# Performance work log

Measured on AMD Instinct MI355X. Metric: run time of the kernel, lower is better.

Reference implementation:

```python
import jax, jax.numpy as jnp
import numpy as np

N, E = 50000, 800000
IN, HID, HEADS, OUT = 128, 32, 8, 40
D1 = HID * HEADS  # 256


def setup_inputs() -> dict:
    key = jax.random.key(0)
    ks = jax.random.split(key, 24)

    def w(k, fin, fout):
        return (jax.random.normal(k, (fin, fout), jnp.float32) / np.sqrt(fin)).astype(jnp.float32)

    def b(k, fout):
        return (jax.random.normal(k, (fout,), jnp.float32) * 0.02).astype(jnp.float32)

    inp = {
        "x": jax.random.normal(ks[0], (N, IN), jnp.float32),
        "edge_index": jax.random.randint(ks[1], (2, E), 0, N, dtype=jnp.int64),
        # layer 1: TransformerConv(IN -> HID, heads=HEADS, concat=True, beta=True)
        "q1w": w(ks[2], IN, D1), "q1b": b(ks[3], D1),
        "k1w": w(ks[4], IN, D1), "k1b": b(ks[5], D1),
        "v1w": w(ks[6], IN, D1), "v1b": b(ks[7], D1),
        "s1w": w(ks[8], IN, D1), "s1b": b(ks[9], D1),
        "b1w": w(ks[10], 3 * D1, 1),
        # layer 2: TransformerConv(D1 -> OUT, heads=1, concat=False, beta=True)
        "q2w": w(ks[11], D1, OUT), "q2b": b(ks[12], OUT),
        "k2w": w(ks[13], D1, OUT), "k2b": b(ks[14], OUT),
        "v2w": w(ks[15], D1, OUT), "v2b": b(ks[16], OUT),
        "s2w": w(ks[17], D1, OUT), "s2b": b(ks[18], OUT),
        "b2w": w(ks[19], 3 * OUT, 1),
    }
    return inp


def _tconv(x, src, dst, qw, qb, kw, kb, vw, vb, sw, sb, bw, heads, ch, concat):
    """PyG TransformerConv (no edge_attr, root_weight=True, beta=True), eval mode."""
    n = x.shape[0]
    q = (x @ qw + qb).reshape(n, heads, ch)
    k = (x @ kw + kb).reshape(n, heads, ch)
    v = (x @ vw + vb).reshape(n, heads, ch)
    # per-edge attention logits: message flows src(j) -> dst(i)
    alpha = jnp.einsum("ehc,ehc->eh", q[dst], k[src]) / np.sqrt(ch)  # [E,H]
    # segment softmax over incoming edges of each dst node
    amax = jax.ops.segment_max(alpha, dst, num_segments=n)  # [N,H]
    a = jnp.exp(alpha - amax[dst])
    asum = jax.ops.segment_sum(a, dst, num_segments=n)  # [N,H]
    attn = a / asum[dst]  # [E,H]
    # scatter-aggregate weighted values
    out = jax.ops.segment_sum(v[src] * attn[:, :, None], dst, num_segments=n)  # [N,H,C]
    out = out.reshape(n, heads * ch) if concat else out.mean(axis=1)
    skip = x @ sw + sb
    beta = jax.nn.sigmoid(jnp.concatenate([out, skip, out - skip], axis=-1) @ bw)  # [N,1]
    return beta * skip + (1.0 - beta) * out


def reference(x, edge_index, q1w, q1b, k1w, k1b, v1w, v1b, s1w, s1b, b1w,
              q2w, q2b, k2w, k2b, v2w, v2b, s2w, s2b, b2w):
    src, dst = edge_index[0], edge_index[1]
    h = jax.nn.elu(_tconv(x, src, dst, q1w, q1b, k1w, k1b, v1w, v1b, s1w, s1b, b1w, HEADS, HID, True))
    return _tconv(h, src, dst, q2w, q2b, k2w, k2b, v2w, v2b, s2w, s2b, b2w, 1, OUT, False)
```

## Files before the change

### kernel.cpp

```cpp
#include <hip/hip_runtime.h>
#include <cstdint>
#include <cstddef>

#define N_NODES 50000
#define N_EDGES 800000
#define IN_F    128
#define HID     32
#define HEADS   8
#define OUT_F   40
#define D1      256
#define W1COLS  1024
#define W2COLS  160
#define CAP     64

#define GFILL_B   3125
#define G1_BX     391
#define G1_BY     8
#define G1_GEMM_B (G1_BX * G1_BY)
#define G1_TOTAL  (GFILL_B + G1_GEMM_B)

typedef unsigned short ushortT;
typedef unsigned char  ucharT;
typedef unsigned short ushortx8 __attribute__((ext_vector_type(8)));
typedef __bf16 bf16x8 __attribute__((ext_vector_type(8)));
typedef float floatx4 __attribute__((ext_vector_type(4)));
typedef float floatx2 __attribute__((ext_vector_type(2)));

__device__ inline ushortT f2bf(float f) {
    union { float f; unsigned int u; } c; c.f = f;
    unsigned int r = c.u + 0x7FFFu + ((c.u >> 16) & 1u);
    return (ushortT)(r >> 16);
}
__device__ inline float bf2f(ushortT h) {
    union { unsigned int u; float f; } c; c.u = ((unsigned int)h) << 16; return c.f;
}

#define PREP_CONV_B  6250
#define PREP_W1_B    512
#define PREP_W2_B    160
#define PREP_TOTAL_B (PREP_CONV_B + PREP_W1_B + PREP_W2_B)

__global__ __launch_bounds__(256) void k_prep(
        const float* __restrict__ x, ushortT* __restrict__ xb,
        const float* __restrict__ q1w, const float* __restrict__ k1w,
        const float* __restrict__ v1w, const float* __restrict__ s1w,
        const float* __restrict__ q1b, const float* __restrict__ k1b,
        const float* __restrict__ v1b, const float* __restrict__ s1b,
        ushortT* __restrict__ W1T, float* __restrict__ b1c,
        const float* __restrict__ q2w, const float* __restrict__ k2w,
        const float* __restrict__ v2w, const float* __restrict__ s2w,
        const float* __restrict__ q2b, const float* __restrict__ k2b,
        const float* __restrict__ v2b, const float* __restrict__ s2b,
        ushortT* __restrict__ W2T, float* __restrict__ b2c) {
    int b = blockIdx.x;
    int tid = threadIdx.x;
    if (b < PREP_CONV_B) {
        int i = b * 256 + tid;
        float4 v = reinterpret_cast<const float4*>(x)[i];
        ushort4 o;
        o.x = f2bf(v.x); o.y = f2bf(v.y); o.z = f2bf(v.z); o.w = f2bf(v.w);
        reinterpret_cast<ushort4*>(xb)[i] = o;
    } else if (b < PREP_CONV_B + PREP_W1_B) {
        int t = (b - PREP_CONV_B) * 256 + tid;
        int c = t / IN_F, k = t % IN_F;
        int sel = c >> 8, cc = c & 255;
        const float* w = sel == 0 ? q1w : sel == 1 ? k1w : sel == 2 ? v1w : s1w;
        W1T[(size_t)c * IN_F + k] = f2bf(w[(size_t)k * D1 + cc]);
        if (k == 0) {
            const float* bb = sel == 0 ? q1b : sel == 1 ? k1b : sel == 2 ? v1b : s1b;
            b1c[c] = bb[cc];
        }
    } else {
        int t = (b - PREP_CONV_B - PREP_W1_B) * 256 + tid;
        int c = t / D1, k = t % D1;
        int sel = c / OUT_F, cc = c % OUT_F;
        const float* w = sel == 0 ? q2w : sel == 1 ? k2w : sel == 2 ? v2w : s2w;
        W2T[(size_t)c * D1 + k] = f2bf(w[(size_t)k * OUT_F + cc]);
        if (k == 0) {
            const float* bb = sel == 0 ? q2b : sel == 1 ? k2b : sel == 2 ? v2b : s2b;
            b2c[c] = bb[cc];
        }
    }
}

template<int MODE>
__global__ __launch_bounds__(256) void gemm_mfma_pack(
        const ushortT* __restrict__ A, const ushortT* __restrict__ BT,
        const float* __restrict__ bias, float* __restrict__ QSf,
        ushortT* __restrict__ QSh, ucharT* __restrict__ KV8,
        ushortT* __restrict__ K2V2,
        const int* __restrict__ ei, int* __restrict__ cursor, int* __restrict__ col,
        int M, int K, int Nn) {
    constexpr int TM = 128, TN = 128, TK = 64, LDP = 72;
    __shared__ ushortT As[TM * LDP];
    __shared__ ushortT Bs[TN * LDP];
    int bx2, by2;
    if (MODE == 1) {
        int t = blockIdx.x;
        int idx;
        bool isFill;
        if (t < 2 * GFILL_B) { isFill = !(t & 1); idx = t >> 1; }
        else                 { isFill = false;    idx = t - GFILL_B; }
        if (isFill) {
            int e = idx * 256 + threadIdx.x;
            if (e < N_EDGES) {
                int dd = ei[N_EDGES + e];
                int p = atomicAdd(&cursor[dd], 1);
                col[dd * CAP + p] = ei[e];
            }
            return;
        }
        bx2 = idx % G1_BX;
        by2 = idx / G1_BX;
    } else {
        bx2 = blockIdx.x;
        by2 = blockIdx.y;
    }
    int tid = threadIdx.x;
    int lane = tid & 63, wave = tid >> 6;
    int bm = bx2 * TM, bn = by2 * TN;
    int wm = (wave & 1) * 64, wn = (wave >> 1) * 64;
    int mrow = lane & 15, g = lane >> 4;
    floatx4 acc[4][4] = {};

    for (int k0 = 0; k0 < K; k0 += TK) {
#pragma unroll
        for (int it = 0; it < 4; ++it) {
            int idx = tid + it * 256;
            int r = idx >> 3, c = (idx & 7) * 8;
            int gm = bm + r;
            ushortx8 val;
            if (gm < M) val = *reinterpret_cast<const ushortx8*>(A + (size_t)gm * K + k0 + c);
            else        val = (ushortx8)0;
            *reinterpret_cast<ushortx8*>(As + r * LDP + c) = val;
        }
#pragma unroll
        for (int it = 0; it < 4; ++it) {
            int idx = tid + it * 256;
            int r = idx >> 3, c = (idx & 7) * 8;
            int gn = bn + r;
            ushortx8 val;
            if (gn < Nn) val = *reinterpret_cast<const ushortx8*>(BT + (size_t)gn * K + k0 + c);
            else         val = (ushortx8)0;
            *reinterpret_cast<ushortx8*>(Bs + r * LDP + c) = val;
        }
        __syncthreads();
#pragma unroll
        for (int kc = 0; kc < TK / 32; ++kc) {
            bf16x8 a[4], b[4];
#pragma unroll
            for (int i = 0; i < 4; ++i)
                a[i] = *reinterpret_cast<const bf16x8*>(As + (wm + i * 16 + mrow) * LDP + kc * 32 + g * 8);
#pragma unroll
            for (int j = 0; j < 4; ++j)
                b[j] = *reinterpret_cast<const bf16x8*>(Bs + (wn + j * 16 + mrow) * LDP + kc * 32 + g * 8);
#pragma unroll
            for (int i = 0; i < 4; ++i)
#pragma unroll
                for (int j = 0; j < 4; ++j)
                    acc[i][j] = __builtin_amdgcn_mfma_f32_16x16x32_bf16(a[i], b[j], acc[i][j], 0, 0, 0);
        }
        __syncthreads();
    }

    if (MODE == 1) {
        float* lds = reinterpret_cast<float*>(As) + wave * 1088;
        int sec = by2 >> 1;
        int ccbase = (by2 & 1) * 128 + wn;
        int cb4 = (lane & 15) * 4;
        int rlo = lane >> 4;
        float4 bv = *reinterpret_cast<const float4*>(bias + by2 * 128 + wn + cb4);
#pragma unroll
        for (int i = 0; i < 4; ++i) {
#pragma unroll
            for (int j = 0; j < 4; ++j)
#pragma unroll
                for (int r = 0; r < 4; ++r)
                    lds[(g * 4 + r) * 68 + j * 16 + mrow] = acc[i][j][r];
#pragma unroll
            for (int it = 0; it < 4; ++it) {
                int row = it * 4 + rlo;
                int gm = bm + wm + i * 16 + row;
                if (gm >= M) continue;
                float4 v = *reinterpret_cast<float4*>(lds + row * 68 + cb4);
                v.x += bv.x; v.y += bv.y; v.z += bv.z; v.w += bv.w;
                int cc = ccbase + cb4;
                if (sec == 0 || sec == 3) {
                    ushort4 h;
                    h.x = f2bf(v.x); h.y = f2bf(v.y); h.z = f2bf(v.z); h.w = f2bf(v.w);
                    ushortT* dst = QSh + (size_t)gm * 512 + (sec == 3 ? 256 : 0) + cc;
                    *reinterpret_cast<ushort4*>(dst) = h;
                } else {
                    unsigned int pk = 0;
                    pk = __builtin_amdgcn_cvt_pk_fp8_f32(v.x, v.y, pk, false);
                    pk = __builtin_amdgcn_cvt_pk_fp8_f32(v.z, v.w, pk, true);
                    ucharT* dst = KV8 + (size_t)gm * 512 + (sec == 2 ? 256 : 0) + cc;
                    *reinterpret_cast<unsigned int*>(dst) = pk;
                }
            }
        }
    } else {
#pragma unroll
        for (int i = 0; i < 4; ++i) {
#pragma unroll
            for (int j = 0; j < 4; ++j) {
                int gn = bn + wn + j * 16 + mrow;
                if (gn >= Nn) continue;
                float bvs = bias[gn];
#pragma unroll
                for (int r = 0; r < 4; ++r) {
                    int gm = bm + wm + i * 16 + g * 4 + r;
                    if (gm >= M) continue;
                    float val = acc[i][j][r] + bvs;
                    int sec = gn / OUT_F, cc = gn % OUT_F;
                    if (sec == 0)      QSf[(size_t)gm * 80 + cc] = val;
                    else if (sec == 1) K2V2[(size_t)gm * 80 + cc] = f2bf(val);
                    else if (sec == 2) K2V2[(size_t)gm * 80 + 40 + cc] = f2bf(val);
                    else               QSf[(size_t)gm * 80 + 40 + cc] = val;
                }
            }
        }
    }
}

__global__ __launch_bounds__(256) void k_edge1(
        const ushortT* __restrict__ QSh, const ucharT* __restrict__ KV8,
        const float* __restrict__ bw,
        const int* __restrict__ degc, const int* __restrict__ col,
        ushortT* __restrict__ H1b) {
    int gid  = blockIdx.x * blockDim.x + threadIdx.x;
    int node = gid >> 6;
    int lane = threadIdx.x & 63;
    if (node >= N_NODES) return;
    const float scale = 0.17677669529663687f;
    ushort4 qh = *reinterpret_cast<const ushort4*>(QSh + (size_t)node * 512 + lane * 4);
    float4 q;
    q.x = bf2f(qh.x) * scale; q.y = bf2f(qh.y) * scale;
    q.z = bf2f(qh.z) * scale; q.w = bf2f(qh.w) * scale;

    float l = 0.f;
    float4 acc = make_float4(0.f, 0.f, 0.f, 0.f);
    int start = node * CAP;
    int d = degc[node];
    int t = 0;
    for (; t + 2 <= d; t += 2) {
        int j0 = col[start + t];
        int j1 = col[start + t + 1];
        const ucharT* row0 = KV8 + (size_t)j0 * 512 + lane * 4;
        const ucharT* row1 = KV8 + (size_t)j1 * 512 + lane * 4;
        unsigned int ku0 = *reinterpret_cast<const unsigned int*>(row0);
        unsigned int vu0 = *reinterpret_cast<const unsigned int*>(row0 + 256);
        unsigned int ku1 = *reinterpret_cast<const unsigned int*>(row1);
        unsigned int vu1 = *reinterpret_cast<const unsigned int*>(row1 + 256);
        floatx2 k0a = __builtin_amdgcn_cvt_pk_f32_fp8(ku0, false);
        floatx2 k0b = __builtin_amdgcn_cvt_pk_f32_fp8(ku0, true);
        floatx2 k1a = __builtin_amdgcn_cvt_pk_f32_fp8(ku1, false);
        floatx2 k1b = __builtin_amdgcn_cvt_pk_f32_fp8(ku1, true);
        float p0 = q.x * k0a[0] + q.y * k0a[1] + q.z * k0b[0] + q.w * k0b[1];
        float p1 = q.x * k1a[0] + q.y * k1a[1] + q.z * k1b[0] + q.w * k1b[1];
        p0 += __shfl_xor(p0, 1);  p1 += __shfl_xor(p1, 1);
        p0 += __shfl_xor(p0, 2);  p1 += __shfl_xor(p1, 2);
        p0 += __shfl_xor(p0, 4);  p1 += __shfl_xor(p1, 4);
        float e0 = __expf(p0);
        float e1 = __expf(p1);
        l += e0 + e1;
        floatx2 v0a = __builtin_amdgcn_cvt_pk_f32_fp8(vu0, false);
        floatx2 v0b = __builtin_amdgcn_cvt_pk_f32_fp8(vu0, true);
        floatx2 v1a = __builtin_amdgcn_cvt_pk_f32_fp8(vu1, false);
        floatx2 v1b = __builtin_amdgcn_cvt_pk_f32_fp8(vu1, true);
        acc.x += e0 * v0a[0] + e1 * v1a[0];
        acc.y += e0 * v0a[1] + e1 * v1a[1];
        acc.z += e0 * v0b[0] + e1 * v1b[0];
        acc.w += e0 * v0b[1] + e1 * v1b[1];
    }
    if (t < d) {
        int j = col[start + t];
        const ucharT* row = KV8 + (size_t)j * 512 + lane * 4;
        unsigned int ku = *reinterpret_cast<const unsigned int*>(row);
        unsigned int vu = *reinterpret_cast<const unsigned int*>(row + 256);
        floatx2 ka = __builtin_amdgcn_cvt_pk_f32_fp8(ku, false);
        floatx2 kb = __builtin_amdgcn_cvt_pk_f32_fp8(ku, true);
        float p0 = q.x * ka[0] + q.y * ka[1] + q.z * kb[0] + q.w * kb[1];
        p0 += __shfl_xor(p0, 1);
        p0 += __shfl_xor(p0, 2);
        p0 += __shfl_xor(p0, 4);
        float e0 = __expf(p0);
        l += e0;
        floatx2 va = __builtin_amdgcn_cvt_pk_f32_fp8(vu, false);
        floatx2 vb = __builtin_amdgcn_cvt_pk_f32_fp8(vu, true);
        acc.x += e0 * va[0];
        acc.y += e0 * va[1];
        acc.z += e0 * vb[0];
        acc.w += e0 * vb[1];
    }
    float inv = (l > 0.f) ? 1.f / l : 0.f;
    float4 o = make_float4(acc.x * inv, acc.y * inv, acc.z * inv, acc.w * inv);
    ushort4 sh = *reinterpret_cast<const ushort4*>(QSh + (size_t)node * 512 + 256 + lane * 4);
    float4 sk;
    sk.x = bf2f(sh.x); sk.y = bf2f(sh.y); sk.z = bf2f(sh.z); sk.w = bf2f(sh.w);
    const int c4 = lane * 4;
    float4 w0 = *reinterpret_cast<const float4*>(bw + c4);
    float4 w1 = *reinterpret_cast<const float4*>(bw + D1 + c4);
    float4 w2 = *reinterpret_cast<const float4*>(bw + 2 * D1 + c4);
    float part = o.x * w0.x + o.y * w0.y + o.z * w0.z + o.w * w0.w
               + sk.x * w1.x + sk.y * w1.y + sk.z * w1.z + sk.w * w1.w
               + (o.x - sk.x) * w2.x + (o.y - sk.y) * w2.y
               + (o.z - sk.z) * w2.z + (o.w - sk.w) * w2.w;
#pragma unroll
    for (int s = 1; s < 64; s <<= 1) part += __shfl_xor(part, s);
    float beta = 1.f / (1.f + __expf(-part));
    float4 h;
    h.x = beta * sk.x + (1.f - beta) * o.x;
    h.y = beta * sk.y + (1.f - beta) * o.y;
    h.z = beta * sk.z + (1.f - beta) * o.z;
    h.w = beta * sk.w + (1.f - beta) * o.w;
    h.x = h.x > 0.f ? h.x : __expf(h.x) - 1.f;
    h.y = h.y > 0.f ? h.y : __expf(h.y) - 1.f;
    h.z = h.z > 0.f ? h.z : __expf(h.z) - 1.f;
    h.w = h.w > 0.f ? h.w : __expf(h.w) - 1.f;
    ushort4 hb;
    hb.x = f2bf(h.x); hb.y = f2bf(h.y); hb.z = f2bf(h.z); hb.w = f2bf(h.w);
    *reinterpret_cast<ushort4*>(H1b + (size_t)node * D1 + c4) = hb;
}

__global__ __launch_bounds__(256) void k_edge2(
        const float* __restrict__ QS, const ushortT* __restrict__ K2V2,
        const float* __restrict__ bw,
        const int* __restrict__ degc, const int* __restrict__ col,
        float* __restrict__ out) {
    __shared__ float        qbuf[4][40];
    __shared__ float        attn[4][64];
    __shared__ int          jb[4][64];
    __shared__ unsigned int ksm[4][64 * 21];
    int gid  = blockIdx.x * blockDim.x + threadIdx.x;
    int node = gid >> 6;
    int wave = threadIdx.x >> 6;
    int lane = threadIdx.x & 63;
    if (node >= N_NODES) return;
    const float scale = 0.15811388300841897f;
    bool act = lane < OUT_F;
    if (act) qbuf[wave][lane] = QS[(size_t)node * 80 + lane] * scale;

    int d = degc[node];
    if (lane < d) jb[wave][lane] = col[node * CAP + lane];

    const unsigned int* Kdw = reinterpret_cast<const unsigned int*>(K2V2);
    int sr = lane / 20;
    int sc = lane - sr * 20;
    for (int r0 = 0; r0 < d; r0 += 3) {
        int rr = r0 + sr;
        if (lane < 60 && rr < d)
            ksm[wave][rr * 21 + sc] = Kdw[(size_t)jb[wave][rr] * 40 + sc];
    }

    float p = 0.f;
    if (lane < d) {
        float s = 0.f;
#pragma unroll
        for (int c = 0; c < 20; ++c) {
            unsigned int kk = ksm[wave][lane * 21 + c];
            s += qbuf[wave][2 * c]     * bf2f((ushortT)(kk & 0xFFFFu))
               + qbuf[wave][2 * c + 1] * bf2f((ushortT)(kk >> 16));
        }
        p = __expf(s);
    }
    attn[wave][lane] = p;
    float l = p;
#pragma unroll
    for (int s = 1; s < 64; s <<= 1) l += __shfl_xor(l, s);

    float acc = 0.f;
    int ln = act ? lane : 0;
    int e = 0;
    for (; e + 4 <= d; e += 4) {
        int je0 = jb[wave][e],     je1 = jb[wave][e + 1];
        int je2 = jb[wave][e + 2], je3 = jb[wave][e + 3];
        float v0 = bf2f(K2V2[(size_t)je0 * 80 + 40 + ln]);
        float v1 = bf2f(K2V2[(size_t)je1 * 80 + 40 + ln]);
        float v2 = bf2f(K2V2[(size_t)je2 * 80 + 40 + ln]);
        float v3 = bf2f(K2V2[(size_t)je3 * 80 + 40 + ln]);
        acc += (attn[wave][e] * v0 + attn[wave][e + 1] * v1)
             + (attn[wave][e + 2] * v2 + attn[wave][e + 3] * v3);
    }
    for (; e < d; ++e)
        acc += attn[wave][e] * bf2f(K2V2[(size_t)jb[wave][e] * 80 + 40 + ln]);

    float inv = (l > 0.f) ? 1.f / l : 0.f;
    float o  = acc * inv;
    float sk = act ? QS[(size_t)node * 80 + 40 + lane] : 0.f;
    float part = act ? (o * bw[lane] + sk * bw[OUT_F + lane] + (o - sk) * bw[2 * OUT_F + lane]) : 0.f;
#pragma unroll
    for (int s = 1; s < 64; s <<= 1) part += __shfl_xor(part, s);
    float beta = 1.f / (1.f + __expf(-part));
    if (act) out[(size_t)node * OUT_F + lane] = beta * sk + (1.f - beta) * o;
}

extern "C" void kernel_launch(void* const* d_in, const int* in_sizes, int n_in,
                              void* d_out, int out_size, void* d_ws, size_t ws_size,
                              hipStream_t stream) {
    const float* x   = (const float*)d_in[0];
    const int*   ei  = (const int*)d_in[1];
    const float* q1w = (const float*)d_in[2];
    const float* q1b = (const float*)d_in[3];
    const float* k1w = (const float*)d_in[4];
    const float* k1b = (const float*)d_in[5];
    const float* v1w = (const float*)d_in[6];
    const float* v1b = (const float*)d_in[7];
    const float* s1w = (const float*)d_in[8];
    const float* s1b = (const float*)d_in[9];
    const float* b1w = (const float*)d_in[10];
    const float* q2w = (const float*)d_in[11];
    const float* q2b = (const float*)d_in[12];
    const float* k2w = (const float*)d_in[13];
    const float* k2b = (const float*)d_in[14];
    const float* v2w = (const float*)d_in[15];
    const float* v2b = (const float*)d_in[16];
    const float* s2w = (const float*)d_in[17];
    const float* s2b = (const float*)d_in[18];
    const float* b2w = (const float*)d_in[19];
    float* out = (float*)d_out;

    char* w = (char*)d_ws;
    ushortT* QSh = (ushortT*)w;
    ucharT*  KV8 = (ucharT*)(w + 51200000);
    ushortT* H1b = (ushortT*)(w + 102400000);
    ushortT* xb  = (ushortT*)(w + 128000000);
    ushortT* W1T = (ushortT*)(w + 140800000);
    ushortT* W2T = (ushortT*)(w + 141062144);
    float*   b1c = (float*)(w + 141144064);
    float*   b2c = (float*)(w + 141148160);
    int* cursor  = (int*)(w + 141149184);
    int* col     = cursor + N_NODES;
    float*   QS2  = (float*)w;
    ushortT* K2V2 = (ushortT*)(w + 51200000);

    hipMemsetAsync(cursor, 0, (size_t)N_NODES * sizeof(int), stream);

    k_prep<<<PREP_TOTAL_B, 256, 0, stream>>>(
        x, xb,
        q1w, k1w, v1w, s1w, q1b, k1b, v1b, s1b, W1T, b1c,
        q2w, k2w, v2w, s2w, q2b, k2b, v2b, s2b, W2T, b2c);

    gemm_mfma_pack<1><<<G1_TOTAL, 256, 0, stream>>>(
        xb, W1T, b1c, nullptr, QSh, KV8, nullptr,
        ei, cursor, col, N_NODES, IN_F, W1COLS);

    k_edge1<<<(N_NODES * 64) / 256, 256, 0, stream>>>(QSh, KV8, b1w, cursor, col, H1b);

    dim3 g2((N_NODES + 127) / 128, (W2COLS + 127) / 128);
    gemm_mfma_pack<2><<<g2, 256, 0, stream>>>(H1b, W2T, b2c, QS2, nullptr, nullptr,
                                              K2V2, nullptr, nullptr, nullptr,
                                              N_NODES, D1, W2COLS);

    k_edge2<<<(N_NODES * 64) / 256, 256, 0, stream>>>(QS2, K2V2, b2w, cursor, col, out);
}
```

Baseline: 376.3 us.

## Load GEMM MFMA operands directly from global memory, drop LDS staging

The GEMM no longer stages A and B tiles through shared memory with block-wide barriers. Each wave now loads its bf16x8 MFMA fragments straight from global memory using per-row pointers clamped to the matrix bounds, and shared memory is kept only for the epilogue transpose buffer. This removes the LDS writes and reads and the __syncthreads, but drops cross-wave reuse, so each operand row is fetched by two waves and relies on L1/L2 hits. The row clamping replaces zero-fill for out-of-range rows.

```diff
diff --git a/kernel.cpp b/kernel.cpp
--- a/kernel.cpp
+++ b/kernel.cpp
@@ -21,7 +21,6 @@
 
 typedef unsigned short ushortT;
 typedef unsigned char  ucharT;
-typedef unsigned short ushortx8 __attribute__((ext_vector_type(8)));
 typedef __bf16 bf16x8 __attribute__((ext_vector_type(8)));
 typedef float floatx4 __attribute__((ext_vector_type(4)));
 typedef float floatx2 __attribute__((ext_vector_type(2)));
@@ -91,9 +90,8 @@
         ushortT* __restrict__ K2V2,
         const int* __restrict__ ei, int* __restrict__ cursor, int* __restrict__ col,
         int M, int K, int Nn) {
-    constexpr int TM = 128, TN = 128, TK = 64, LDP = 72;
-    __shared__ ushortT As[TM * LDP];
-    __shared__ ushortT Bs[TN * LDP];
+    constexpr int TM = 128, TN = 128;
+    __shared__ float tbuf[4 * 1088];
     int bx2, by2;
     if (MODE == 1) {
         int t = blockIdx.x;
@@ -121,50 +119,38 @@
     int bm = bx2 * TM, bn = by2 * TN;
     int wm = (wave & 1) * 64, wn = (wave >> 1) * 64;
     int mrow = lane & 15, g = lane >> 4;
+
+    const ushortT* Ab[4];
+    const ushortT* Bb[4];
+#pragma unroll
+    for (int i = 0; i < 4; ++i) {
+        int gm = bm + wm + i * 16 + mrow;
+        if (gm > M - 1) gm = M - 1;
+        Ab[i] = A + (size_t)gm * K + g * 8;
+    }
+#pragma unroll
+    for (int j = 0; j < 4; ++j) {
+        int gn = bn + wn + j * 16 + mrow;
+        if (gn > Nn - 1) gn = Nn - 1;
+        Bb[j] = BT + (size_t)gn * K + g * 8;
+    }
+
     floatx4 acc[4][4] = {};
-
-    for (int k0 = 0; k0 < K; k0 += TK) {
-#pragma unroll
-        for (int it = 0; it < 4; ++it) {
-            int idx = tid + it * 256;
-            int r = idx >> 3, c = (idx & 7) * 8;
-            int gm = bm + r;
-            ushortx8 val;
-            if (gm < M) val = *reinterpret_cast<const ushortx8*>(A + (size_t)gm * K + k0 + c);
-            else        val = (ushortx8)0;
-            *reinterpret_cast<ushortx8*>(As + r * LDP + c) = val;
-        }
-#pragma unroll
-        for (int it = 0; it < 4; ++it) {
-            int idx = tid + it * 256;
-            int r = idx >> 3, c = (idx & 7) * 8;
-            int gn = bn + r;
-            ushortx8 val;
-            if (gn < Nn) val = *reinterpret_cast<const ushortx8*>(BT + (size_t)gn * K + k0 + c);
-            else         val = (ushortx8)0;
-            *reinterpret_cast<ushortx8*>(Bs + r * LDP + c) = val;
-        }
-        __syncthreads();
-#pragma unroll
-        for (int kc = 0; kc < TK / 32; ++kc) {
-            bf16x8 a[4], b[4];
-#pragma unroll
-            for (int i = 0; i < 4; ++i)
-                a[i] = *reinterpret_cast<const bf16x8*>(As + (wm + i * 16 + mrow) * LDP + kc * 32 + g * 8);
+    for (int k0 = 0; k0 < K; k0 += 32) {
+        bf16x8 a[4], b[4];
+#pragma unroll
+        for (int i = 0; i < 4; ++i) { a[i] = *reinterpret_cast<const bf16x8*>(Ab[i]); Ab[i] += 32; }
+#pragma unroll
+        for (int j = 0; j < 4; ++j) { b[j] = *reinterpret_cast<const bf16x8*>(Bb[j]); Bb[j] += 32; }
+#pragma unroll
+        for (int i = 0; i < 4; ++i)
 #pragma unroll
             for (int j = 0; j < 4; ++j)
-                b[j] = *reinterpret_cast<const bf16x8*>(Bs + (wn + j * 16 + mrow) * LDP + kc * 32 + g * 8);
-#pragma unroll
-            for (int i = 0; i < 4; ++i)
-#pragma unroll
-                for (int j = 0; j < 4; ++j)
-                    acc[i][j] = __builtin_amdgcn_mfma_f32_16x16x32_bf16(a[i], b[j], acc[i][j], 0, 0, 0);
-        }
-        __syncthreads();
+                acc[i][j] = __builtin_amdgcn_mfma_f32_16x16x32_bf16(a[i], b[j], acc[i][j], 0, 0, 0);
     }
 
     if (MODE == 1) {
-        float* lds = reinterpret_cast<float*>(As) + wave * 1088;
+        float* lds = tbuf + wave * 1088;
         int sec = by2 >> 1;
         int ccbase = (by2 & 1) * 128 + wn;
         int cb4 = (lane & 15) * 4;
```

After: 399.5 us. 6.2% more time.

## Fold cursor zeroing into prep kernel and shrink GEMM K-tile to raise occupancy

Applied to the files above, without the earlier changes.

The separate hipMemsetAsync launch is removed, and the cursor array is now zeroed by extra blocks inside k_prep, saving one launch. The GEMM K tile drops from 64 to 32 with a narrower LDS pitch, and both tiles share one buffer. This roughly halves shared memory per block so more blocks fit per CU, at the cost of twice as many k-iterations and barriers. The epilogue staging, which needs 4*1088 floats, still fits in the smaller buffer.

```diff
diff --git a/kernel.cpp b/kernel.cpp
--- a/kernel.cpp
+++ b/kernel.cpp
@@ -35,12 +35,14 @@
     union { unsigned int u; float f; } c; c.u = ((unsigned int)h) << 16; return c.f;
 }
 
+#define PREP_Z_B     196
 #define PREP_CONV_B  6250
 #define PREP_W1_B    512
 #define PREP_W2_B    160
-#define PREP_TOTAL_B (PREP_CONV_B + PREP_W1_B + PREP_W2_B)
+#define PREP_TOTAL_B (PREP_Z_B + PREP_CONV_B + PREP_W1_B + PREP_W2_B)
 
 __global__ __launch_bounds__(256) void k_prep(
+        int* __restrict__ cursor,
         const float* __restrict__ x, ushortT* __restrict__ xb,
         const float* __restrict__ q1w, const float* __restrict__ k1w,
         const float* __restrict__ v1w, const float* __restrict__ s1w,
@@ -54,14 +56,17 @@
         ushortT* __restrict__ W2T, float* __restrict__ b2c) {
     int b = blockIdx.x;
     int tid = threadIdx.x;
-    if (b < PREP_CONV_B) {
+    if (b < PREP_Z_B) {
         int i = b * 256 + tid;
+        if (i < N_NODES) cursor[i] = 0;
+    } else if (b < PREP_Z_B + PREP_CONV_B) {
+        int i = (b - PREP_Z_B) * 256 + tid;
         float4 v = reinterpret_cast<const float4*>(x)[i];
         ushort4 o;
         o.x = f2bf(v.x); o.y = f2bf(v.y); o.z = f2bf(v.z); o.w = f2bf(v.w);
         reinterpret_cast<ushort4*>(xb)[i] = o;
-    } else if (b < PREP_CONV_B + PREP_W1_B) {
-        int t = (b - PREP_CONV_B) * 256 + tid;
+    } else if (b < PREP_Z_B + PREP_CONV_B + PREP_W1_B) {
+        int t = (b - PREP_Z_B - PREP_CONV_B) * 256 + tid;
         int c = t / IN_F, k = t % IN_F;
         int sel = c >> 8, cc = c & 255;
         const float* w = sel == 0 ? q1w : sel == 1 ? k1w : sel == 2 ? v1w : s1w;
@@ -71,7 +76,7 @@
             b1c[c] = bb[cc];
         }
     } else {
-        int t = (b - PREP_CONV_B - PREP_W1_B) * 256 + tid;
+        int t = (b - PREP_Z_B - PREP_CONV_B - PREP_W1_B) * 256 + tid;
         int c = t / D1, k = t % D1;
         int sel = c / OUT_F, cc = c % OUT_F;
         const float* w = sel == 0 ? q2w : sel == 1 ? k2w : sel == 2 ? v2w : s2w;
@@ -91,9 +96,10 @@
         ushortT* __restrict__ K2V2,
         const int* __restrict__ ei, int* __restrict__ cursor, int* __restrict__ col,
         int M, int K, int Nn) {
-    constexpr int TM = 128, TN = 128, TK = 64, LDP = 72;
-    __shared__ ushortT As[TM * LDP];
-    __shared__ ushortT Bs[TN * LDP];
+    constexpr int TM = 128, TN = 128, TK = 32, LDP = 40;
+    __shared__ ushortT smem[TM * LDP + TN * LDP];
+    ushortT* As = smem;
+    ushortT* Bs = smem + TM * LDP;
     int bx2, by2;
     if (MODE == 1) {
         int t = blockIdx.x;
@@ -125,9 +131,9 @@
 
     for (int k0 = 0; k0 < K; k0 += TK) {
 #pragma unroll
-        for (int it = 0; it < 4; ++it) {
+        for (int it = 0; it < 2; ++it) {
             int idx = tid + it * 256;
-            int r = idx >> 3, c = (idx & 7) * 8;
+            int r = idx >> 2, c = (idx & 3) * 8;
             int gm = bm + r;
             ushortx8 val;
             if (gm < M) val = *reinterpret_cast<const ushortx8*>(A + (size_t)gm * K + k0 + c);
@@ -135,9 +141,9 @@
             *reinterpret_cast<ushortx8*>(As + r * LDP + c) = val;
         }
 #pragma unroll
-        for (int it = 0; it < 4; ++it) {
+        for (int it = 0; it < 2; ++it) {
             int idx = tid + it * 256;
-            int r = idx >> 3, c = (idx & 7) * 8;
+            int r = idx >> 2, c = (idx & 3) * 8;
             int gn = bn + r;
             ushortx8 val;
             if (gn < Nn) val = *reinterpret_cast<const ushortx8*>(BT + (size_t)gn * K + k0 + c);
@@ -145,15 +151,14 @@
             *reinterpret_cast<ushortx8*>(Bs + r * LDP + c) = val;
         }
         __syncthreads();
-#pragma unroll
-        for (int kc = 0; kc < TK / 32; ++kc) {
+        {
             bf16x8 a[4], b[4];
 #pragma unroll
             for (int i = 0; i < 4; ++i)
-                a[i] = *reinterpret_cast<const bf16x8*>(As + (wm + i * 16 + mrow) * LDP + kc * 32 + g * 8);
+                a[i] = *reinterpret_cast<const bf16x8*>(As + (wm + i * 16 + mrow) * LDP + g * 8);
 #pragma unroll
             for (int j = 0; j < 4; ++j)
-                b[j] = *reinterpret_cast<const bf16x8*>(Bs + (wn + j * 16 + mrow) * LDP + kc * 32 + g * 8);
+                b[j] = *reinterpret_cast<const bf16x8*>(Bs + (wn + j * 16 + mrow) * LDP + g * 8);
 #pragma unroll
             for (int i = 0; i < 4; ++i)
 #pragma unroll
@@ -164,7 +169,7 @@
     }
 
     if (MODE == 1) {
-        float* lds = reinterpret_cast<float*>(As) + wave * 1088;
+        float* lds = reinterpret_cast<float*>(smem) + wave * 1088;
         int sec = by2 >> 1;
         int ccbase = (by2 & 1) * 128 + wn;
         int cb4 = (lane & 15) * 4;
@@ -434,10 +439,8 @@
     float*   QS2  = (float*)w;
     ushortT* K2V2 = (ushortT*)(w + 51200000);
 
-    hipMemsetAsync(cursor, 0, (size_t)N_NODES * sizeof(int), stream);
-
     k_prep<<<PREP_TOTAL_B, 256, 0, stream>>>(
-        x, xb,
+        cursor, x, xb,
         q1w, k1w, v1w, s1w, q1b, k1b, v1b, s1b, W1T, b1c,
         q2w, k2w, v2w, s2w, q2b, k2b, v2b, s2b, W2T, b2c);
 
```

Measured after the change: 357.3 us. 1.05x faster.
